# Kernel optimization log

Measured on AMD Instinct MI355X. Metric: run time of the kernel, lower is better.

The kernel has to match this reference:

```python
import jax, jax.numpy as jnp
import numpy as np

B, T, C = 2, 2048, 2048
N_HEAD, N_KV_HEAD = 16, 4
HEAD_DIM = C // N_HEAD          # 128
N_REP = N_HEAD // N_KV_HEAD    # 4
WINDOW = 512


def setup_inputs() -> dict:
    key = jax.random.key(0)
    k1, k2, k3 = jax.random.split(key, 3)
    x = jax.random.normal(k1, (B, T, C), dtype=jnp.float32)
    w_attn = jax.random.normal(k2, (C, (N_HEAD + 2 * N_KV_HEAD) * HEAD_DIM), dtype=jnp.float32) * 0.02
    w_proj = jax.random.normal(k3, (C, C), dtype=jnp.float32) * 0.02
    # RoPE cos/sin table: [T, HEAD_DIM//2, 2]
    inv_freq = 1.0 / (10000.0 ** (jnp.arange(0, HEAD_DIM, 2, dtype=jnp.float32) / HEAD_DIM))
    ang = jnp.arange(T, dtype=jnp.float32)[:, None] * inv_freq[None, :]
    freqs_cis = jnp.stack([jnp.cos(ang), jnp.sin(ang)], axis=-1)
    mask = jnp.ones((T, T), dtype=bool)  # True = masked (except window, forced allowed)
    return {"x": x, "w_attn": w_attn, "w_proj": w_proj, "freqs_cis": freqs_cis, "mask": mask}


def _apply_rope(t, freqs_cis):
    # t: [B, T, H, D]; freqs_cis: [T, D//2, 2] (cos, sin)
    b, s, h, d = t.shape
    tp = t.reshape(b, s, h, d // 2, 2)
    cos = freqs_cis[:, None, :, 0]  # [T,1,D/2]
    sin = freqs_cis[:, None, :, 1]
    tr = tp[..., 0] * cos - tp[..., 1] * sin
    ti = tp[..., 0] * sin + tp[..., 1] * cos
    return jnp.stack([tr, ti], axis=-1).reshape(b, s, h, d)


def reference(x, w_attn, w_proj, freqs_cis, mask):
    qkv = x @ w_attn  # [B,T,(H+2KV)*D]
    q_size = N_HEAD * HEAD_DIM
    kv_size = N_KV_HEAD * HEAD_DIM
    q = qkv[..., :q_size].reshape(B, T, N_HEAD, HEAD_DIM)
    k = qkv[..., q_size:q_size + kv_size].reshape(B, T, N_KV_HEAD, HEAD_DIM)
    v = qkv[..., q_size + kv_size:].reshape(B, T, N_KV_HEAD, HEAD_DIM)
    q = _apply_rope(q, freqs_cis)
    k = _apply_rope(k, freqs_cis)
    # GQA repeat_kv
    k = jnp.repeat(k, N_REP, axis=2)
    v = jnp.repeat(v, N_REP, axis=2)
    q = q.transpose(0, 2, 1, 3)  # [B,H,T,D]
    k = k.transpose(0, 2, 1, 3)
    v = v.transpose(0, 2, 1, 3)
    # effective mask: window positions forced allowed, rest per input mask
    i = jnp.arange(T)[:, None]
    j = jnp.arange(T)[None, :]
    in_window = (j <= i) & (i - j < WINDOW)
    effective = mask & ~in_window  # True = masked (-inf)
    scores = jnp.einsum("bhqd,bhkd->bhqk", q, k) / jnp.sqrt(jnp.float32(HEAD_DIM))
    scores = jnp.where(effective[None, None], -jnp.inf, scores)
    attn = jax.nn.softmax(scores, axis=-1)
    y = jnp.einsum("bhqk,bhkd->bhqd", attn, v)
    y = y.transpose(0, 2, 1, 3).reshape(B, T, C)
    return y @ w_proj
```

## Files before the change

kernel.cpp:

```cpp
#include <hip/hip_runtime.h>
#include <hip/hip_bf16.h>

typedef __attribute__((ext_vector_type(8))) short short8;
typedef __attribute__((ext_vector_type(4))) float f32x4;

#define MFMA16(a,b,c) __builtin_amdgcn_mfma_f32_16x16x32_bf16((a),(b),(c),0,0,0)

static __device__ __forceinline__ unsigned short f2b(float f){
  __hip_bfloat16 h = __float2bfloat16(f);
  return __builtin_bit_cast(unsigned short, h);
}
static __device__ __forceinline__ float b2f(unsigned short u){
  unsigned int v = ((unsigned int)u)<<16;
  return __builtin_bit_cast(float, v);
}

static __device__ __forceinline__ void gld_lds16(const void* g, void* l){
  __builtin_amdgcn_global_load_lds((const __attribute__((address_space(1))) unsigned int*)g,
                                   (__attribute__((address_space(3))) unsigned int*)l, 16, 0, 0);
}

__global__ __launch_bounds__(256) void k_prep(const float* __restrict__ x,
    const float* __restrict__ wA, const float* __restrict__ wP,
    unsigned short* __restrict__ xb, unsigned short* __restrict__ wtA,
    unsigned short* __restrict__ wtP){
  int bid = blockIdx.x, tid = threadIdx.x;
  if (bid < 4096){
    int i = (bid*256 + tid)*8;
    float4 a = *(const float4*)(x+i);
    float4 b = *(const float4*)(x+i+4);
    short8 v;
    v[0]=f2b(a.x); v[1]=f2b(a.y); v[2]=f2b(a.z); v[3]=f2b(a.w);
    v[4]=f2b(b.x); v[5]=f2b(b.y); v[6]=f2b(b.z); v[7]=f2b(b.w);
    *(short8*)(xb+i) = v;
    return;
  }
  __shared__ float tile[32][33];
  const float* in; unsigned short* out; int R, C, bx, by;
  if (bid < 10240){ int tt = bid-4096;  in=wA; out=wtA; R=2048; C=3072; bx=tt%96; by=tt/96; }
  else            { int tt = bid-10240; in=wP; out=wtP; R=2048; C=2048; bx=tt%64; by=tt/64; }
  int c0 = bx*32, r0 = by*32;
  int tx = tid&31, ty = tid>>5;
  #pragma unroll
  for (int i=0;i<4;i++) tile[ty*4+i][tx] = in[(size_t)(r0+ty*4+i)*C + c0+tx];
  __syncthreads();
  #pragma unroll
  for (int i=0;i<4;i++) out[(size_t)(c0+ty*4+i)*R + r0+tx] = f2b(tile[tx][ty*4+i]);
}

template<int OB>
__global__ __launch_bounds__(256,2) void k_gemm97(const unsigned short* __restrict__ A,
    const unsigned short* __restrict__ BT, void* __restrict__ Cv,
    int M, int N, int K, int nbx){
  __shared__ __align__(16) unsigned short As[128*64];
  __shared__ __align__(16) unsigned short Bs[128*64];
  const int NT = K >> 6;
  int cpx = gridDim.x >> 3;
  int bid = blockIdx.x;
  int swz = (bid & 7)*cpx + (bid >> 3);
  int bm = (swz / nbx)*128, bn = (swz % nbx)*128;
  int tid = threadIdx.x;
  int wave = tid >> 6, lane = tid & 63;
  int r = lane & 15, g = lane >> 4;
  int wr = (wave >> 1)*64, wc = (wave & 1)*64;
  int sw = r & 7;

  f32x4 acc[4][4];
  #pragma unroll
  for (int i=0;i<4;i++)
    #pragma unroll
    for (int j=0;j<4;j++){ acc[i][j][0]=0.f; acc[i][j][1]=0.f; acc[i][j][2]=0.f; acc[i][j][3]=0.f; }

  for (int t=0; t<NT; ++t){
    #pragma unroll
    for (int i=0;i<4;i++){
      int c = i*256 + tid;
      int row = c>>3, kc = c&7;
      gld_lds16(&A[(size_t)(bm+row)*K + (size_t)t*64 + ((kc^(row&7))*8)], (char*)As + c*16);
    }
    #pragma unroll
    for (int i=0;i<4;i++){
      int c = i*256 + tid;
      int row = c>>3, kc = c&7;
      gld_lds16(&BT[(size_t)(bn+row)*K + (size_t)t*64 + ((kc^(row&7))*8)], (char*)Bs + c*16);
    }
    __syncthreads();
    short8 af[4][2], bf[4][2];
    #pragma unroll
    for (int i=0;i<4;i++)
      #pragma unroll
      for (int kk=0;kk<2;kk++){
        int row = wr + i*16 + r;
        af[i][kk] = *(const short8*)((const char*)As + ((size_t)(row*8 + ((kk*4+g)^sw))<<4));
      }
    #pragma unroll
    for (int j=0;j<4;j++)
      #pragma unroll
      for (int kk=0;kk<2;kk++){
        int row = wc + j*16 + r;
        bf[j][kk] = *(const short8*)((const char*)Bs + ((size_t)(row*8 + ((kk*4+g)^sw))<<4));
      }
    #pragma unroll
    for (int kk=0;kk<2;kk++)
      #pragma unroll
      for (int i=0;i<4;i++)
        #pragma unroll
        for (int j=0;j<4;j++)
          acc[i][j] = MFMA16(af[i][kk], bf[j][kk], acc[i][j]);
    __syncthreads();
  }

  #pragma unroll
  for (int i=0;i<4;i++)
    #pragma unroll
    for (int j=0;j<4;j++)
      #pragma unroll
      for (int rr=0;rr<4;rr++){
        size_t idx = (size_t)(bm + wr + i*16 + 4*g + rr)*N + bn + wc + j*16 + r;
        if (OB) ((unsigned short*)Cv)[idx] = f2b(acc[i][j][rr]);
        else    ((float*)Cv)[idx] = acc[i][j][rr];
      }
}

__global__ __launch_bounds__(256) void k_rope_split(const unsigned short* __restrict__ qkv,
    const float* __restrict__ fc, unsigned short* __restrict__ qb,
    unsigned short* __restrict__ kb){
  int row = blockIdx.x;
  int t = row & 2047, b = row >> 11;
  int tid = threadIdx.x;
  const unsigned short* qr = qkv + (size_t)row*3072;
  const float QS = 0.12751743f;
  #pragma unroll
  for (int ii=0; ii<4; ii++){
    int p = tid + 256*ii;
    int h = p>>6, f = p&63;
    unsigned int pr = *(const unsigned int*)&qr[h*128 + 2*f];
    float x0 = b2f((unsigned short)(pr & 0xffff)), x1 = b2f((unsigned short)(pr >> 16));
    float2 cssn = *(const float2*)&fc[t*128 + 2*f];
    float o0 = (x0*cssn.x - x1*cssn.y)*QS, o1 = (x0*cssn.y + x1*cssn.x)*QS;
    size_t o = ((size_t)(b*16 + h)*2048 + t)*128 + 2*f;
    qb[o] = f2b(o0); qb[o+1] = f2b(o1);
  }
  {
    int p = tid; int kh = p>>6, f = p&63;
    unsigned int pr = *(const unsigned int*)&qr[2048 + kh*128 + 2*f];
    float x0 = b2f((unsigned short)(pr & 0xffff)), x1 = b2f((unsigned short)(pr >> 16));
    float2 cssn = *(const float2*)&fc[t*128 + 2*f];
    float o0 = x0*cssn.x - x1*cssn.y, o1 = x0*cssn.y + x1*cssn.x;
    size_t o = ((size_t)(b*4 + kh)*2048 + t)*128 + 2*f;
    kb[o] = f2b(o0); kb[o+1] = f2b(o1);
  }
}

__global__ void k_transpose_v(const unsigned short* __restrict__ qkv,
                              unsigned short* __restrict__ vt){
  __shared__ unsigned short tile[32][33];
  int bk = blockIdx.z;
  int d0 = blockIdx.x*32, t0 = blockIdx.y*32;
  int tx = threadIdx.x, ty = threadIdx.y;
  const unsigned short* vp = qkv + (size_t)(bk>>2)*2048*3072 + 2560 + (bk&3)*128;
  unsigned short* vtp = vt + (size_t)bk*128*2048;
  #pragma unroll
  for (int i=0;i<4;i++) tile[ty*4+i][tx] = vp[(size_t)(t0+ty*4+i)*3072 + d0+tx];
  __syncthreads();
  #pragma unroll
  for (int i=0;i<4;i++) vtp[(size_t)(d0+ty*4+i)*2048 + t0+tx] = tile[tx][ty*4+i];
}

__global__ __launch_bounds__(256,2) void k_attn(const unsigned short* __restrict__ q,
    const unsigned short* __restrict__ k, const unsigned short* __restrict__ vt,
    unsigned short* __restrict__ y){
  int qb0 = blockIdx.x*128;
  int h = blockIdx.y, b = blockIdx.z;
  int kvh = h>>2;
  int tid = threadIdx.x, wave = tid>>6, lane = tid&63;
  int w0A = qb0 + wave*32, w0B = w0A + 16;
  int r = lane&15, g = lane>>4;
  const unsigned short* qh = q + ((size_t)(b*16+h)*2048)*128;
  const unsigned short* kh = k + ((size_t)(b*4+kvh)*2048)*128;
  const unsigned short* vh = vt + ((size_t)(b*4+kvh)*128)*2048;

  __shared__ unsigned short Ks[2][64*128];
  __shared__ unsigned short Vs[2][128*64];
  __shared__ unsigned short plds[4][16][76];

  short8 qfA[4], qfB[4];
  #pragma unroll
  for (int c=0;c<4;c++){
    qfA[c] = *(const short8*)&qh[(w0A+r)*128 + c*32 + g*8];
    qfB[c] = *(const short8*)&qh[(w0B+r)*128 + c*32 + g*8];
  }

  f32x4 accA[8], accB[8];
  #pragma unroll
  for (int d=0; d<8; d++){
    accA[d][0]=0.f; accA[d][1]=0.f; accA[d][2]=0.f; accA[d][3]=0.f;
    accB[d][0]=0.f; accB[d][1]=0.f; accB[d][2]=0.f; accB[d][3]=0.f;
  }
  float mA[4]  = {-1e30f,-1e30f,-1e30f,-1e30f};
  float mB[4]  = {-1e30f,-1e30f,-1e30f,-1e30f};
  float lsA[4] = {0.f,0.f,0.f,0.f};
  float lsB[4] = {0.f,0.f,0.f,0.f};

  int lo = qb0 - 511; if (lo < 0) lo = 0;
  int t0 = lo & ~63;
  int nt = ((qb0 + 127) - t0)/64 + 1;
  int sw = (r&7)<<4;

  #define STAGE(bb, kt)                                                          \
    { _Pragma("unroll")                                                          \
      for (int p=0;p<4;p++){                                                     \
        int c = p*256 + tid;                                                     \
        int row = c>>4, col = (c&15)*16;                                         \
        gld_lds16((const char*)kh + (size_t)((kt)+row)*256 + (col ^ ((row&7)<<4)),\
                  (char*)&Ks[bb][0] + c*16);                                     \
      }                                                                          \
      _Pragma("unroll")                                                          \
      for (int p=0;p<4;p++){                                                     \
        int c = p*256 + tid;                                                     \
        int row = c>>3, col = (c&7)*16;                                          \
        gld_lds16((const char*)vh + (size_t)row*4096 + (size_t)(kt)*2 + (col ^ ((row&7)<<4)),\
                  (char*)&Vs[bb][0] + c*16);                                     \
      }                                                                          \
    }

  STAGE(0, t0);
  __syncthreads();
  int cur = 0;

  for (int it=0; it<nt; it++){
    int kt = t0 + it*64;
    if (it+1 < nt) STAGE(cur^1, kt + 64);

    bool useA = (kt <= w0A+15) && (kt+63 >= w0A-511);
    bool useB = (kt <= w0B+15) && (kt+63 >= w0B-511);
    if (useA || useB){
      f32x4 SA[4], SB[4];
      __builtin_amdgcn_s_setprio(1);
      #pragma unroll
      for (int s=0;s<4;s++){
        f32x4 aA; aA[0]=0.f; aA[1]=0.f; aA[2]=0.f; aA[3]=0.f;
        f32x4 aB; aB[0]=0.f; aB[1]=0.f; aB[2]=0.f; aB[3]=0.f;
        const char* kr = (const char*)&Ks[cur][0] + (s*16+r)*256;
        #pragma unroll
        for (int c=0;c<4;c++){
          short8 kf = *(const short8*)(kr + ((c*64 + g*16) ^ sw));
          aA = MFMA16(qfA[c], kf, aA);
          aB = MFMA16(qfB[c], kf, aB);
        }
        SA[s] = aA; SB[s] = aB;
      }
      __builtin_amdgcn_s_setprio(0);
      bool fullA = (kt+63 <= w0A) && (kt >= w0A-496);
      bool fullB = (kt+63 <= w0B) && (kt >= w0B-496);
      float lmA[4], lmB[4];
      if (fullA){
        #pragma unroll
        for (int rr=0;rr<4;rr++)
          lmA[rr] = fmaxf(fmaxf(SA[0][rr],SA[1][rr]), fmaxf(SA[2][rr],SA[3][rr]));
      } else {
        #pragma unroll
        for (int rr=0;rr<4;rr++){
          int baseA = w0A + 4*g + rr - kt;
          float ma = -3e38f;
          #pragma unroll
          for (int s=0;s<4;s++){
            int dd = baseA - s*16 - r;
            float sa = ((unsigned)dd < 512u) ? SA[s][rr] : -3e38f;
            SA[s][rr] = sa;
            ma = fmaxf(ma, sa);
          }
          lmA[rr] = ma;
        }
      }
      if (fullB){
        #pragma unroll
        for (int rr=0;rr<4;rr++)
          lmB[rr] = fmaxf(fmaxf(SB[0][rr],SB[1][rr]), fmaxf(SB[2][rr],SB[3][rr]));
      } else {
        #pragma unroll
        for (int rr=0;rr<4;rr++){
          int baseB = w0B + 4*g + rr - kt;
          float mb_ = -3e38f;
          #pragma unroll
          for (int s=0;s<4;s++){
            int dd = baseB - s*16 - r;
            float sb = ((unsigned)dd < 512u) ? SB[s][rr] : -3e38f;
            SB[s][rr] = sb;
            mb_ = fmaxf(mb_, sb);
          }
          lmB[rr] = mb_;
        }
      }
      bool okA = true, okB = true;
      #pragma unroll
      for (int rr=0;rr<4;rr++){
        okA = okA && (lmA[rr] - mA[rr] <= 8.f);
        okB = okB && (lmB[rr] - mB[rr] <= 8.f);
      }
      if (!__all(okA)){
        float mxA[4];
        #pragma unroll
        for (int rr=0;rr<4;rr++) mxA[rr] = lmA[rr];
        #pragma unroll
        for (int st=1; st<16; st<<=1)
          #pragma unroll
          for (int rr=0;rr<4;rr++)
            mxA[rr] = fmaxf(mxA[rr], __shfl_xor(mxA[rr], st));
        #pragma unroll
        for (int rr=0;rr<4;rr++){
          float mn = fmaxf(mA[rr], mxA[rr]);
          float al = exp2f(mA[rr] - mn);
          mA[rr] = mn;
          lsA[rr] *= al;
          #pragma unroll
          for (int d=0;d<8;d++) accA[d][rr] *= al;
        }
      }
      if (!__all(okB)){
        float mxB[4];
        #pragma unroll
        for (int rr=0;rr<4;rr++) mxB[rr] = lmB[rr];
        #pragma unroll
        for (int st=1; st<16; st<<=1)
          #pragma unroll
          for (int rr=0;rr<4;rr++)
            mxB[rr] = fmaxf(mxB[rr], __shfl_xor(mxB[rr], st));
        #pragma unroll
        for (int rr=0;rr<4;rr++){
          float mn = fmaxf(mB[rr], mxB[rr]);
          float al = exp2f(mB[rr] - mn);
          mB[rr] = mn;
          lsB[rr] *= al;
          #pragma unroll
          for (int d=0;d<8;d++) accB[d][rr] *= al;
        }
      }
      #pragma unroll
      for (int rr=0;rr<4;rr++){
        float psA = 0.f, psB = 0.f;
        #pragma unroll
        for (int s=0;s<4;s++){
          float pa = exp2f(SA[s][rr] - mA[rr]);
          float pb = exp2f(SB[s][rr] - mB[rr]);
          SA[s][rr] = pa; SB[s][rr] = pb;
          psA += pa; psB += pb;
        }
        lsA[rr] += psA;
        lsB[rr] += psB;
      }
      #pragma unroll
      for (int rr=0;rr<4;rr++)
        #pragma unroll
        for (int s=0;s<4;s++)
          plds[wave][4*g+rr][s*16+r] = f2b(SA[s][rr]);
      short8 pfA0 = *(const short8*)&plds[wave][r][g*8];
      short8 pfA1 = *(const short8*)&plds[wave][r][32 + g*8];
      #pragma unroll
      for (int rr=0;rr<4;rr++)
        #pragma unroll
        for (int s=0;s<4;s++)
          plds[wave][4*g+rr][s*16+r] = f2b(SB[s][rr]);
      short8 pfB0 = *(const short8*)&plds[wave][r][g*8];
      short8 pfB1 = *(const short8*)&plds[wave][r][32 + g*8];
      __builtin_amdgcn_s_setprio(1);
      #pragma unroll
      for (int d=0;d<8;d++){
        const char* vr = (const char*)&Vs[cur][0] + (d*16+r)*128;
        short8 vf0 = *(const short8*)(vr + ((g*16) ^ sw));
        short8 vf1 = *(const short8*)(vr + ((64 + g*16) ^ sw));
        accA[d] = MFMA16(pfA0, vf0, accA[d]);
        accA[d] = MFMA16(pfA1, vf1, accA[d]);
        accB[d] = MFMA16(pfB0, vf0, accB[d]);
        accB[d] = MFMA16(pfB1, vf1, accB[d]);
      }
      __builtin_amdgcn_s_setprio(0);
    }
    __syncthreads();
    cur ^= 1;
  }

  #pragma unroll
  for (int rr=0;rr<4;rr++){
    float sa = lsA[rr], sb = lsB[rr];
    #pragma unroll
    for (int st=1; st<16; st<<=1){ sa += __shfl_xor(sa, st); sb += __shfl_xor(sb, st); }
    float invA = 1.f/sa, invB = 1.f/sb;
    int iA = w0A + 4*g + rr, iB = w0B + 4*g + rr;
    #pragma unroll
    for (int d=0;d<8;d++){
      y[((size_t)(b*2048)+iA)*2048 + h*128 + d*16 + r] = f2b(accA[d][rr]*invA);
      y[((size_t)(b*2048)+iB)*2048 + h*128 + d*16 + r] = f2b(accB[d][rr]*invB);
    }
  }
}

extern "C" void kernel_launch(void* const* d_in, const int* in_sizes, int n_in,
                              void* d_out, int out_size, void* d_ws, size_t ws_size,
                              hipStream_t stream) {
  const float* x      = (const float*)d_in[0];
  const float* w_attn = (const float*)d_in[1];
  const float* w_proj = (const float*)d_in[2];
  const float* fc     = (const float*)d_in[3];
  float* out = (float*)d_out;
  char* ws = (char*)d_ws;
  unsigned short* xb   = (unsigned short*)(ws);
  unsigned short* wtA  = (unsigned short*)(ws + 16777216);
  unsigned short* wtP  = (unsigned short*)(ws + 29360128);
  unsigned short* qkvb = (unsigned short*)(ws + 37748736);
  unsigned short* yb   = (unsigned short*)(ws + 37748736);
  unsigned short* qb   = (unsigned short*)(ws + 62914560);
  unsigned short* kb   = (unsigned short*)(ws + 79691776);
  unsigned short* vtb  = (unsigned short*)(ws + 83886080);

  k_prep<<<14336, 256, 0, stream>>>(x, w_attn, w_proj, xb, wtA, wtP);
  k_gemm97<1><<<dim3(768), 256, 0, stream>>>(xb, wtA, qkvb, 4096, 3072, 2048, 24);
  k_rope_split<<<4096, 256, 0, stream>>>(qkvb, fc, qb, kb);
  k_transpose_v<<<dim3(4,64,8), dim3(32,8), 0, stream>>>(qkvb, vtb);
  k_attn<<<dim3(16,16,2), 256, 0, stream>>>(qb, kb, vtb, yb);
  k_gemm97<0><<<dim3(512), 256, 0, stream>>>(yb, wtP, out, 4096, 2048, 2048, 16);
}
```

Before: 167.5 us.

## Fuse Q RoPE into attention and merge K-rope with V transpose kernel

```diff
diff --git a/kernel.cpp b/kernel.cpp
--- a/kernel.cpp
+++ b/kernel.cpp
@@ -122,42 +122,28 @@
       }
 }
 
-__global__ __launch_bounds__(256) void k_rope_split(const unsigned short* __restrict__ qkv,
-    const float* __restrict__ fc, unsigned short* __restrict__ qb,
-    unsigned short* __restrict__ kb){
-  int row = blockIdx.x;
-  int t = row & 2047, b = row >> 11;
-  int tid = threadIdx.x;
-  const unsigned short* qr = qkv + (size_t)row*3072;
-  const float QS = 0.12751743f;
-  #pragma unroll
-  for (int ii=0; ii<4; ii++){
-    int p = tid + 256*ii;
-    int h = p>>6, f = p&63;
-    unsigned int pr = *(const unsigned int*)&qr[h*128 + 2*f];
-    float x0 = b2f((unsigned short)(pr & 0xffff)), x1 = b2f((unsigned short)(pr >> 16));
-    float2 cssn = *(const float2*)&fc[t*128 + 2*f];
-    float o0 = (x0*cssn.x - x1*cssn.y)*QS, o1 = (x0*cssn.y + x1*cssn.x)*QS;
-    size_t o = ((size_t)(b*16 + h)*2048 + t)*128 + 2*f;
-    qb[o] = f2b(o0); qb[o+1] = f2b(o1);
-  }
-  {
-    int p = tid; int kh = p>>6, f = p&63;
-    unsigned int pr = *(const unsigned int*)&qr[2048 + kh*128 + 2*f];
+__global__ __launch_bounds__(256) void k_mid(const unsigned short* __restrict__ qkv,
+    const float* __restrict__ fc, unsigned short* __restrict__ kb,
+    unsigned short* __restrict__ vt){
+  int bid = blockIdx.x, tid = threadIdx.x;
+  if (bid < 4096){
+    int row = bid;
+    int t = row & 2047, b = row >> 11;
+    const unsigned short* qr = qkv + (size_t)row*3072 + 2048;
+    int kh = tid>>6, f = tid&63;
+    unsigned int pr = *(const unsigned int*)&qr[kh*128 + 2*f];
     float x0 = b2f((unsigned short)(pr & 0xffff)), x1 = b2f((unsigned short)(pr >> 16));
     float2 cssn = *(const float2*)&fc[t*128 + 2*f];
     float o0 = x0*cssn.x - x1*cssn.y, o1 = x0*cssn.y + x1*cssn.x;
     size_t o = ((size_t)(b*4 + kh)*2048 + t)*128 + 2*f;
     kb[o] = f2b(o0); kb[o+1] = f2b(o1);
-  }
-}
-
-__global__ void k_transpose_v(const unsigned short* __restrict__ qkv,
-                              unsigned short* __restrict__ vt){
+    return;
+  }
   __shared__ unsigned short tile[32][33];
-  int bk = blockIdx.z;
-  int d0 = blockIdx.x*32, t0 = blockIdx.y*32;
-  int tx = threadIdx.x, ty = threadIdx.y;
+  int tt = bid - 4096;
+  int xx = tt & 3, yy = (tt>>2) & 63, bk = tt >> 8;
+  int d0 = xx*32, t0 = yy*32;
+  int tx = tid & 31, ty = tid >> 5;
   const unsigned short* vp = qkv + (size_t)(bk>>2)*2048*3072 + 2560 + (bk&3)*128;
   unsigned short* vtp = vt + (size_t)bk*128*2048;
   #pragma unroll
@@ -167,16 +153,16 @@
   for (int i=0;i<4;i++) vtp[(size_t)(d0+ty*4+i)*2048 + t0+tx] = tile[tx][ty*4+i];
 }
 
-__global__ __launch_bounds__(256,2) void k_attn(const unsigned short* __restrict__ q,
-    const unsigned short* __restrict__ k, const unsigned short* __restrict__ vt,
-    unsigned short* __restrict__ y){
+__global__ __launch_bounds__(256,2) void k_attn(const unsigned short* __restrict__ qkv,
+    const float* __restrict__ fc, const unsigned short* __restrict__ k,
+    const unsigned short* __restrict__ vt, unsigned short* __restrict__ y){
   int qb0 = blockIdx.x*128;
   int h = blockIdx.y, b = blockIdx.z;
   int kvh = h>>2;
   int tid = threadIdx.x, wave = tid>>6, lane = tid&63;
   int w0A = qb0 + wave*32, w0B = w0A + 16;
   int r = lane&15, g = lane>>4;
-  const unsigned short* qh = q + ((size_t)(b*16+h)*2048)*128;
+  const unsigned short* qsrc = qkv + (size_t)(b*2048)*3072 + h*128;
   const unsigned short* kh = k + ((size_t)(b*4+kvh)*2048)*128;
   const unsigned short* vh = vt + ((size_t)(b*4+kvh)*128)*2048;
 
@@ -184,11 +170,31 @@
   __shared__ unsigned short Vs[2][128*64];
   __shared__ unsigned short plds[4][16][76];
 
+  const float QS = 0.12751743f;
   short8 qfA[4], qfB[4];
-  #pragma unroll
-  for (int c=0;c<4;c++){
-    qfA[c] = *(const short8*)&qh[(w0A+r)*128 + c*32 + g*8];
-    qfB[c] = *(const short8*)&qh[(w0B+r)*128 + c*32 + g*8];
+  {
+    int tA = w0A + r, tB = w0B + r;
+    const float* fcA = fc + (size_t)tA*128;
+    const float* fcB = fc + (size_t)tB*128;
+    #pragma unroll
+    for (int c=0;c<4;c++){
+      int d0 = c*32 + g*8;
+      short8 rawA = *(const short8*)&qsrc[(size_t)tA*3072 + d0];
+      short8 rawB = *(const short8*)&qsrc[(size_t)tB*3072 + d0];
+      short8 oA, oB;
+      #pragma unroll
+      for (int j=0;j<4;j++){
+        float a0 = b2f((unsigned short)rawA[2*j]), a1 = b2f((unsigned short)rawA[2*j+1]);
+        float b0 = b2f((unsigned short)rawB[2*j]), b1 = b2f((unsigned short)rawB[2*j+1]);
+        float2 csA = *(const float2*)&fcA[d0 + 2*j];
+        float2 csB = *(const float2*)&fcB[d0 + 2*j];
+        oA[2*j]   = (short)f2b((a0*csA.x - a1*csA.y)*QS);
+        oA[2*j+1] = (short)f2b((a0*csA.y + a1*csA.x)*QS);
+        oB[2*j]   = (short)f2b((b0*csB.x - b1*csB.y)*QS);
+        oB[2*j+1] = (short)f2b((b0*csB.y + b1*csB.x)*QS);
+      }
+      qfA[c] = oA; qfB[c] = oB;
+    }
   }
 
   f32x4 accA[8], accB[8];
@@ -408,15 +414,13 @@
   unsigned short* wtA  = (unsigned short*)(ws + 16777216);
   unsigned short* wtP  = (unsigned short*)(ws + 29360128);
   unsigned short* qkvb = (unsigned short*)(ws + 37748736);
-  unsigned short* yb   = (unsigned short*)(ws + 37748736);
-  unsigned short* qb   = (unsigned short*)(ws + 62914560);
+  unsigned short* yb   = (unsigned short*)(ws + 62914560);
   unsigned short* kb   = (unsigned short*)(ws + 79691776);
   unsigned short* vtb  = (unsigned short*)(ws + 83886080);
 
   k_prep<<<14336, 256, 0, stream>>>(x, w_attn, w_proj, xb, wtA, wtP);
   k_gemm97<1><<<dim3(768), 256, 0, stream>>>(xb, wtA, qkvb, 4096, 3072, 2048, 24);
-  k_rope_split<<<4096, 256, 0, stream>>>(qkvb, fc, qb, kb);
-  k_transpose_v<<<dim3(4,64,8), dim3(32,8), 0, stream>>>(qkvb, vtb);
-  k_attn<<<dim3(16,16,2), 256, 0, stream>>>(qb, kb, vtb, yb);
+  k_mid<<<6144, 256, 0, stream>>>(qkvb, fc, kb, vtb);
+  k_attn<<<dim3(16,16,2), 256, 0, stream>>>(qkvb, fc, kb, vtb, yb);
   k_gemm97<0><<<dim3(512), 256, 0, stream>>>(yb, wtP, out, 4096, 2048, 2048, 16);
 }
```

Measured after the change: 164.4 us, median of 2. About the same (-1.9%).
